# Performance work log

Hardware: AMD Instinct MI355X
Metric: run time of the kernel (lower is better)

The kernel has to match this reference:

```python
import jax, jax.numpy as jnp
import numpy as np

MASK_VALUE = -10000.0


def setup_inputs() -> dict:
    key = jax.random.key(0)
    ks = jax.random.split(key, 6)
    F_, H, L1N, L2N, B = 1024, 2048, 64, 256, 8192

    def w(k, shape, fan_in):
        return jax.random.normal(k, shape, jnp.float32) * (1.0 / np.sqrt(fan_in))

    x = jax.random.normal(ks[0], (B, F_), jnp.float32)
    W1_1 = w(ks[1], (F_, H), F_); b1_1 = jnp.zeros((H,), jnp.float32)
    W1_2 = w(ks[2], (H, L1N), H); b1_2 = jnp.zeros((L1N,), jnp.float32)
    W2_1 = w(ks[3], (F_, H), F_); b2_1 = jnp.zeros((H,), jnp.float32)
    W2_2 = w(ks[4], (2 * H, L2N), 2 * H); b2_2 = jnp.zeros((L2N,), jnp.float32)
    # child_parent[j] = L1 parent of L2 label j (contiguous groups of 4),
    # equivalent to L12_table = [[4i,4i+1,4i+2,4i+3] for i in range(64)]
    child_parent = jnp.arange(L2N, dtype=jnp.int32) // (L2N // L1N)
    return dict(x=x, W1_1=W1_1, b1_1=b1_1, W1_2=W1_2, b1_2=b1_2,
                W2_1=W2_1, b2_1=b2_1, W2_2=W2_2, b2_2=b2_2,
                child_parent=child_parent)


def reference(x, W1_1, b1_1, W1_2, b1_2, W2_1, b2_1, W2_2, b2_2, child_parent):
    h1 = jax.nn.relu(x @ W1_1 + b1_1)          # [B, H]
    h2 = jax.nn.relu(x @ W2_1 + b2_1)          # [B, H]
    cat = jnp.concatenate([h1, h2], axis=1)    # [B, 2H]
    L1 = jax.nn.softmax(jax.nn.relu(h1 @ W1_2 + b1_2), axis=1)   # [B, L1N]
    l2_logits = jax.nn.relu(cat @ W2_2 + b2_2)                   # [B, L2N]
    parent = jnp.argmax(L1, axis=1)                              # [B] int
    # mask[i, j] = 0 if L2 label j is a child of argmax L1 label, else MASK_VALUE
    mask = jnp.where(child_parent[None, :] == parent[:, None], 0.0, MASK_VALUE)
    L2 = jax.nn.softmax(l2_logits + mask, axis=1)
    return (L1, L2)
```

## Files before the change

kernel.cpp:

```cpp
#include <hip/hip_runtime.h>
#include <hip/hip_bf16.h>
#include <stdint.h>
#include <math.h>


typedef _Float16 f16x8 __attribute__((ext_vector_type(8)));
typedef _Float16 f16x4 __attribute__((ext_vector_type(4)));
typedef float    f32x4 __attribute__((ext_vector_type(4)));
typedef unsigned short u16x4 __attribute__((ext_vector_type(4)));

#define MASK_VALUE (-10000.0f)
#define SWZ(r) ((((r) + ((r) >> 2))) & 3)
#define SW4(row, c) ((c) ^ (((row) >> 1) & 3))
#define RSCALE 2048.0f
#define INV_RSCALE (1.0f / 2048.0f)

#define GLOBAL_AS __attribute__((address_space(1)))
#define LDS_AS    __attribute__((address_space(3)))

__device__ __forceinline__ void gload16(const void* g, void* lds) {
    __builtin_amdgcn_global_load_lds((const GLOBAL_AS void*)g, (LDS_AS void*)lds, 16, 0, 0);
}

__device__ __forceinline__ float rd_any(const void* p, size_t i, int flag) {
    return flag ? (float)((const __hip_bfloat16*)p)[i] : ((const float*)p)[i];
}

__device__ __forceinline__ void wg_bar() {
    asm volatile("" ::: "memory");
    __builtin_amdgcn_s_barrier();
    asm volatile("" ::: "memory");
}
#define LGKMN(n) do { asm volatile("s_waitcnt lgkmcnt(" #n ")" ::: "memory"); \
                      __builtin_amdgcn_sched_barrier(0); } while (0)
#define VMW(n)  asm volatile("s_waitcnt vmcnt(" #n ")" ::: "memory")
#define SB0()   __builtin_amdgcn_sched_barrier(0)
#define MFMA16(a,b,c) __builtin_amdgcn_mfma_f32_16x16x32_f16((a),(b),(c),0,0,0)

__global__ void detect_dtype(const unsigned int* __restrict__ x, int* __restrict__ flag) {
    __shared__ int cnt;
    if (threadIdx.x == 0) cnt = 0;
    __syncthreads();
    int local = 0;
#pragma unroll
    for (int i = 0; i < 4; ++i) {
        unsigned int w = x[threadIdx.x * 4 + i];
        unsigned int e = (w >> 7) & 0xFFu;
        if (e >= 96u && e <= 144u) local++;
    }
    atomicAdd(&cnt, local);
    __syncthreads();
    if (threadIdx.x == 0) *flag = (cnt >= 600) ? 1 : 0;
}

__global__ void prep_all(
    const void* __restrict__ x, const void* __restrict__ W1_1,
    const void* __restrict__ W2_1, const void* __restrict__ W2_2,
    const void* __restrict__ W1_2,
    _Float16* __restrict__ xh, _Float16* __restrict__ xl,
    _Float16* __restrict__ whT, _Float16* __restrict__ wlT,
    _Float16* __restrict__ W2Tf, _Float16* __restrict__ W22Tf,
    _Float16* __restrict__ w12h, _Float16* __restrict__ w12l,
    const int* __restrict__ flagp)
{
    __shared__ __align__(16) float tile[64][65];
    int flag = *flagp;
    int bid = blockIdx.x, t = threadIdx.x;
    int tx = t & 63, ty = t >> 6;

    if (bid < 8192) {
        size_t i = ((size_t)bid * 256 + t) * 4;
        float a0, a1, a2, a3;
        if (flag) {
            u16x4 u = *(const u16x4*)((const unsigned short*)x + i);
            a0 = __uint_as_float(((unsigned)u[0]) << 16);
            a1 = __uint_as_float(((unsigned)u[1]) << 16);
            a2 = __uint_as_float(((unsigned)u[2]) << 16);
            a3 = __uint_as_float(((unsigned)u[3]) << 16);
        } else {
            f32x4 f = *(const f32x4*)((const float*)x + i);
            a0 = f[0]; a1 = f[1]; a2 = f[2]; a3 = f[3];
        }
        f16x4 hv, lv;
        _Float16 h0 = (_Float16)a0; hv[0] = h0; lv[0] = (_Float16)((a0 - (float)h0) * RSCALE);
        _Float16 h1 = (_Float16)a1; hv[1] = h1; lv[1] = (_Float16)((a1 - (float)h1) * RSCALE);
        _Float16 h2 = (_Float16)a2; hv[2] = h2; lv[2] = (_Float16)((a2 - (float)h2) * RSCALE);
        _Float16 h3 = (_Float16)a3; hv[3] = h3; lv[3] = (_Float16)((a3 - (float)h3) * RSCALE);
        *(f16x4*)(xh + i) = hv;
        *(f16x4*)(xl + i) = lv;
        return;
    }

    if (bid < 8704) {
        int b = bid - 8192;
        int c0 = (b & 31) * 64, r0 = (b >> 5) * 64;
#pragma unroll
        for (int i = 0; i < 16; ++i) {
            int r = ty + i * 4;
            tile[r][tx] = rd_any(W1_1, (size_t)(r0 + r) * 2048 + c0 + tx, flag);
        }
        __syncthreads();
#pragma unroll
        for (int i = 0; i < 16; ++i) {
            int r = ty + i * 4;
            size_t o = (size_t)(c0 + r) * 1024 + r0 + tx;
            float a = tile[tx][r];
            _Float16 h = (_Float16)a;
            whT[o] = h;
            wlT[o] = (_Float16)((a - (float)h) * RSCALE);
        }
        return;
    }

    if (bid < 9216) {
        int b = bid - 8704;
        int c0 = (b & 31) * 64, r0 = (b >> 5) * 64;
#pragma unroll
        for (int i = 0; i < 16; ++i) {
            int r = ty + i * 4;
            tile[r][tx] = rd_any(W2_1, (size_t)(r0 + r) * 2048 + c0 + tx, flag);
        }
        __syncthreads();
#pragma unroll
        for (int i = 0; i < 16; ++i) {
            int r = ty + i * 4;
            W2Tf[(size_t)(c0 + r) * 1024 + r0 + tx] = (_Float16)tile[tx][r];
        }
        return;
    }

    if (bid < 9472) {
        int b = bid - 9216;
        int c0 = (b & 3) * 64, r0 = (b >> 2) * 64;
#pragma unroll
        for (int i = 0; i < 16; ++i) {
            int r = ty + i * 4;
            tile[r][tx] = rd_any(W2_2, (size_t)(r0 + r) * 256 + c0 + tx, flag);
        }
        __syncthreads();
#pragma unroll
        for (int i = 0; i < 16; ++i) {
            int r = ty + i * 4;
            W22Tf[(size_t)(c0 + r) * 4096 + r0 + tx] = (_Float16)tile[tx][r];
        }
        return;
    }

    {
        int b = bid - 9472;
        int r0 = b * 64;
#pragma unroll
        for (int i = 0; i < 16; ++i) {
            int r = ty + i * 4;
            tile[r][tx] = rd_any(W1_2, (size_t)(r0 + r) * 64 + tx, flag);
        }
        __syncthreads();
#pragma unroll
        for (int i = 0; i < 16; ++i) {
            int r = ty + i * 4;
            size_t o = (size_t)r * 2048 + r0 + tx;
            float a = tile[tx][r];
            _Float16 h = (_Float16)a;
            w12h[o] = h;
            w12l[o] = (_Float16)((a - (float)h) * RSCALE);
        }
    }
}

__global__ __launch_bounds__(512, 2) void h12_gemm8(
    const _Float16* __restrict__ xh, const _Float16* __restrict__ xl,
    const _Float16* __restrict__ whT, const _Float16* __restrict__ wlT,
    const void* __restrict__ b11,
    const _Float16* __restrict__ W2Tf, const void* __restrict__ b21,
    _Float16* __restrict__ h1h, _Float16* __restrict__ h1l,
    _Float16* __restrict__ h2b,
    const int* __restrict__ flagp)
{
    __shared__ __align__(16) char smem[147456];
    int flag = *flagp;
    int t = threadIdx.x, w = t >> 6, lane = t & 63;
    int ml = lane & 15, q = lane >> 4, rq = q * 4;

    int xcd = blockIdx.x & 7, rblk = blockIdx.x >> 3;

    if (rblk < 64) {
        int lb = xcd * 64 + rblk;
        int mt = lb >> 4, nt = lb & 15;
        int i0 = mt * 256, j0 = nt * 128;
        int wr = w & 3, wc = w >> 2;

        f32x4 acc1[4][4], acc2[4][4];
#pragma unroll
        for (int a = 0; a < 4; ++a)
#pragma unroll
            for (int b = 0; b < 4; ++b) {
                acc1[a][b] = (f32x4){0.f, 0.f, 0.f, 0.f};
                acc2[a][b] = (f32x4){0.f, 0.f, 0.f, 0.f};
            }

        f16x8 ah[4], al[4], bh[4], bl[4];

        auto stage = [&](char* bp, int kt, int g) {
            if (g < 4) {
                int ci = ((g & 1) << 9) + t;
                int row = ci >> 2;
                int c = SW4(row, ci & 3);
                const _Float16* src = (g < 2) ? xh : xl;
                gload16(src + (size_t)(i0 + row) * 1024 + kt + c * 8,
                        bp + ((g < 2) ? 0 : 16384) + ci * 16);
            } else {
                int ci = t;
                int row = ci >> 2;
                int c = SW4(row, ci & 3);
                const _Float16* src = (g == 4) ? whT : wlT;
                gload16(src + (size_t)(j0 + row) * 1024 + kt + c * 8,
                        bp + ((g == 4) ? 32768 : 40960) + ci * 16);
            }
        };
        auto rdBA = [&](char* bp) {
#pragma unroll
            for (int ct = 0; ct < 2; ++ct) {
                int row = wc * 64 + ct * 16 + ml;
                int off = row * 64 + (SW4(row, q) << 4);
                bh[ct] = *(const f16x8*)(bp + 32768 + off);
                bl[ct] = *(const f16x8*)(bp + 40960 + off);
            }
        };
        auto rdBB = [&](char* bp) {
#pragma unroll
            for (int ct = 2; ct < 4; ++ct) {
                int row = wc * 64 + ct * 16 + ml;
                int off = row * 64 + (SW4(row, q) << 4);
                bh[ct] = *(const f16x8*)(bp + 32768 + off);
                bl[ct] = *(const f16x8*)(bp + 40960 + off);
            }
        };
        auto rdAlow = [&](char* bp) {
#pragma unroll
            for (int rt = 0; rt < 2; ++rt) {
                int row = wr * 64 + rt * 16 + ml;
                int off = row * 64 + (SW4(row, q) << 4);
                ah[rt] = *(const f16x8*)(bp + off);
                al[rt] = *(const f16x8*)(bp + 16384 + off);
            }
        };
        auto rdAhigh = [&](char* bp) {
#pragma unroll
            for (int rt = 2; rt < 4; ++rt) {
                int row = wr * 64 + rt * 16 + ml;
                int off = row * 64 + (SW4(row, q) << 4);
                ah[rt] = *(const f16x8*)(bp + off);
                al[rt] = *(const f16x8*)(bp + 16384 + off);
            }
        };

#pragma unroll
        for (int g = 0; g < 6; ++g) stage(smem, 0, g);
#pragma unroll
        for (int g = 0; g < 6; ++g) stage(smem + 49152, 32, g);
        VMW(6);
        wg_bar();
        rdBA(smem);   SB0();
        rdAlow(smem); SB0();
        rdBB(smem);   SB0();

        int cur = 0;
        for (int s = 0; s < 32; ++s) {
            char* bpc = smem + cur * 49152;
            char* bpn = smem + ((cur + 1 == 3) ? 0 : cur + 1) * 49152;
            int cur2 = cur + 2; if (cur2 >= 3) cur2 -= 3;
            char* bp2 = smem + cur2 * 49152;
            int kt2 = (s + 2) * 32;
            bool st = (s < 30), rd = (s < 31);

            if (st) {
#pragma unroll
                for (int g = 0; g < 6; ++g) stage(bp2, kt2, g);
            }
            rdAhigh(bpc);
            LGKMN(4);
            __builtin_amdgcn_s_setprio(1);
#pragma unroll
            for (int rt = 0; rt < 2; ++rt)
#pragma unroll
                for (int ct = 0; ct < 4; ++ct) {
                    acc1[rt][ct] = MFMA16(ah[rt], bh[ct], acc1[rt][ct]);
                    acc2[rt][ct] = MFMA16(ah[rt], bl[ct], acc2[rt][ct]);
                    acc2[rt][ct] = MFMA16(al[rt], bh[ct], acc2[rt][ct]);
                }
            __builtin_amdgcn_s_setprio(0);
            LGKMN(0);
            __builtin_amdgcn_s_setprio(1);
#pragma unroll
            for (int rt = 2; rt < 4; ++rt)
#pragma unroll
                for (int ct = 0; ct < 2; ++ct) {
                    acc1[rt][ct] = MFMA16(ah[rt], bh[ct], acc1[rt][ct]);
                    acc2[rt][ct] = MFMA16(ah[rt], bl[ct], acc2[rt][ct]);
                    acc2[rt][ct] = MFMA16(al[rt], bh[ct], acc2[rt][ct]);
                }
            __builtin_amdgcn_s_setprio(0);
            if (st) { VMW(6); } else { VMW(0); }
            wg_bar();
            if (rd) { rdBA(bpn); rdAlow(bpn); }
            SB0();
            __builtin_amdgcn_s_setprio(1);
#pragma unroll
            for (int rt = 2; rt < 4; ++rt)
#pragma unroll
                for (int ct = 2; ct < 4; ++ct) {
                    acc1[rt][ct] = MFMA16(ah[rt], bh[ct], acc1[rt][ct]);
                    acc2[rt][ct] = MFMA16(ah[rt], bl[ct], acc2[rt][ct]);
                    acc2[rt][ct] = MFMA16(al[rt], bh[ct], acc2[rt][ct]);
                }
            __builtin_amdgcn_s_setprio(0);
            if (rd) rdBB(bpn);
            SB0();
            cur = cur + 1; if (cur == 3) cur = 0;
        }

#pragma unroll
        for (int ct = 0; ct < 4; ++ct) {
            float bv = rd_any(b11, j0 + wc * 64 + ct * 16 + ml, flag);
#pragma unroll
            for (int rt = 0; rt < 4; ++rt)
#pragma unroll
                for (int rr = 0; rr < 4; ++rr) {
                    float v = acc1[rt][ct][rr] + acc2[rt][ct][rr] * INV_RSCALE + bv;
                    acc1[rt][ct][rr] = v > 0.f ? v : 0.f;
                }
        }
        _Float16* C = (_Float16*)smem;
#pragma unroll
        for (int p = 0; p < 2; ++p) {
            __syncthreads();
#pragma unroll
            for (int rt = 0; rt < 4; ++rt)
#pragma unroll
                for (int ct = 0; ct < 4; ++ct)
#pragma unroll
                    for (int rr = 0; rr < 4; ++rr) {
                        float v = acc1[rt][ct][rr];
                        _Float16 h = (_Float16)v;
                        _Float16 outv = (p == 0) ? h
                                      : (_Float16)((v - (float)h) * RSCALE);
                        int rl = wr * 64 + rt * 16 + rq + rr;
                        int cl = wc * 64 + ct * 16 + ml;
                        C[rl * 136 + cl] = outv;
                    }
            __syncthreads();
            _Float16* dst = (p == 0) ? h1h : h1l;
#pragma unroll
            for (int i = 0; i < 8; ++i) {
                int c = i * 512 + t;
                int row = c >> 4, c8 = (c & 15) * 8;
                *(f16x8*)(dst + (size_t)(i0 + row) * 2048 + j0 + c8) =
                    *(const f16x8*)(C + row * 136 + c8);
            }
        }
    } else {
        int lb = xcd * 32 + (rblk - 64);
        int mt = lb >> 3, nt = lb & 7;
        int i0 = mt * 256, j0 = nt * 256;
        int wr = w & 1, wc = w >> 1;

        f32x4 acc[8][4];
#pragma unroll
        for (int a = 0; a < 8; ++a)
#pragma unroll
            for (int b = 0; b < 4; ++b) acc[a][b] = (f32x4){0.f, 0.f, 0.f, 0.f};

        f16x8 af0[4], af4[4], bfa[4], bfb[4];

        auto stage = [&](char* bp, int kt, int g) {
            int ci = ((g & 1) << 9) + t;
            int row = ci >> 2;
            int c = SW4(row, ci & 3);
            if (g < 2)
                gload16(xh + (size_t)(i0 + row) * 1024 + kt + c * 8,
                        bp + ci * 16);
            else
                gload16(W2Tf + (size_t)(j0 + row) * 1024 + kt + c * 8,
                        bp + 16384 + ci * 16);
        };
        auto rdBF = [&](char* bp, f16x8* dst) {
#pragma unroll
            for (int ct = 0; ct < 4; ++ct) {
                int row = wc * 64 + ct * 16 + ml;
                int off = row * 64 + (SW4(row, q) << 4);
                dst[ct] = *(const f16x8*)(bp + 16384 + off);
            }
        };
        auto rdA0 = [&](char* bp) {
#pragma unroll
            for (int rt = 0; rt < 4; ++rt) {
                int row = wr * 128 + rt * 16 + ml;
                int off = row * 64 + (SW4(row, q) << 4);
                af0[rt] = *(const f16x8*)(bp + off);
            }
        };
        auto rdA4 = [&](char* bp) {
#pragma unroll
            for (int rt = 0; rt < 4; ++rt) {
                int row = wr * 128 + (rt + 4) * 16 + ml;
                int off = row * 64 + (SW4(row, q) << 4);
                af4[rt] = *(const f16x8*)(bp + off);
            }
        };

#pragma unroll
        for (int g = 0; g < 4; ++g) stage(smem, 0, g);
#pragma unroll
        for (int g = 0; g < 4; ++g) stage(smem + 32768, 32, g);
        VMW(4);
        wg_bar();
        rdBF(smem, bfa); SB0();
        rdA0(smem);      SB0();
        rdA4(smem);      SB0();

        int cur = 0;
        auto body = [&](int s, f16x8* BFC, f16x8* BFN) {
            char* bpn = smem + ((cur + 1) & 3) * 32768;
            char* bp2 = smem + ((cur + 2) & 3) * 32768;
            int kt2 = (s + 2) * 32;
            bool st = (s < 30), rd = (s < 31);

            if (st) {
#pragma unroll
                for (int g = 0; g < 4; ++g) stage(bp2, kt2, g);
            }
            LGKMN(4);
            __builtin_amdgcn_s_setprio(1);
#pragma unroll
            for (int rt = 0; rt < 4; ++rt)
#pragma unroll
                for (int ct = 0; ct < 4; ++ct)
                    acc[rt][ct] = MFMA16(af0[rt], BFC[ct], acc[rt][ct]);
            __builtin_amdgcn_s_setprio(0);
            LGKMN(0);
            if (st) { VMW(4); } else { VMW(0); }
            wg_bar();
            if (rd) { rdBF(bpn, BFN); rdA0(bpn); }
            SB0();
            __builtin_amdgcn_s_setprio(1);
#pragma unroll
            for (int rt = 0; rt < 4; ++rt)
#pragma unroll
                for (int ct = 0; ct < 4; ++ct)
                    acc[rt + 4][ct] = MFMA16(af4[rt], BFC[ct], acc[rt + 4][ct]);
            __builtin_amdgcn_s_setprio(0);
            if (rd) rdA4(bpn);
            cur = (cur + 1) & 3;
        };

        for (int k = 0; k < 16; ++k) {
            body(2 * k,     bfa, bfb);
            body(2 * k + 1, bfb, bfa);
        }

        _Float16* C = (_Float16*)smem;
        __syncthreads();
#pragma unroll
        for (int ct = 0; ct < 4; ++ct) {
            float bv = rd_any(b21, j0 + wc * 64 + ct * 16 + ml, flag);
#pragma unroll
            for (int rt = 0; rt < 8; ++rt)
#pragma unroll
                for (int rr = 0; rr < 4; ++rr) {
                    float v = acc[rt][ct][rr] + bv;
                    v = v > 0.f ? v : 0.f;
                    int rl = wr * 128 + rt * 16 + rq + rr;
                    int cl = wc * 64 + ct * 16 + ml;
                    C[rl * 264 + cl] = (_Float16)v;
                }
        }
        __syncthreads();
#pragma unroll
        for (int i = 0; i < 16; ++i) {
            int c = i * 512 + t;
            int row = c >> 5, c8 = (c & 31) * 8;
            *(f16x8*)(h2b + (size_t)(i0 + row) * 2048 + j0 + c8) =
                *(const f16x8*)(C + row * 264 + c8);
        }
    }
}

__global__ __launch_bounds__(256, 2) void head_fused(
    const _Float16* __restrict__ h1h, const _Float16* __restrict__ h1l,
    const _Float16* __restrict__ h2b, const _Float16* __restrict__ W22T,
    float* __restrict__ partials,
    const _Float16* __restrict__ w12h, const _Float16* __restrict__ w12l,
    const void* __restrict__ b12, float* __restrict__ L1out,
    int* __restrict__ parent, const int* __restrict__ flagp)
{
    constexpr int BK = 32;
    __shared__ __align__(16) char smem[16384];
    int flag = *flagp;
    int t = threadIdx.x, w = t >> 6, lane = t & 63;
    int ml = lane & 15, q = lane >> 4;

    if (blockIdx.x < 512) {
        _Float16* As = (_Float16*)smem;
        _Float16* Bs = (_Float16*)(smem + 8192);
        int bid = blockIdx.x;
        int g = bid & 7, s = bid >> 3;
        int mt = g * 8 + (s & 7);
        int rest = s >> 3;
        int nt = rest & 1, kc = rest >> 1;
        int i0 = mt * 128, j0 = nt * 128;
        const _Float16* Abase = (kc < 2) ? h1h : h2b;
        int kof = (kc & 1) * 1024;
        int wr = w & 1, wcb = w >> 1;

        f32x4 acc[4][4];
#pragma unroll
        for (int a = 0; a < 4; ++a)
#pragma unroll
            for (int b = 0; b < 4; ++b) acc[a][b] = (f32x4){0.f, 0.f, 0.f, 0.f};

        for (int kt = 0; kt < 1024; kt += BK) {
            __syncthreads();
#pragma unroll
            for (int qq = 0; qq < 2; ++qq) {
                int c = qq * 256 + t;
                int row = c >> 2;
                int gc = (c & 3) ^ SWZ(row);
                gload16(Abase + (size_t)(i0 + row) * 2048 + kof + kt + gc * 8, (char*)As + c * 16);
                gload16(W22T + (size_t)(j0 + row) * 4096 + kc * 1024 + kt + gc * 8, (char*)Bs + c * 16);
            }
            __syncthreads();
            f16x8 af[4], bf[4];
#pragma unroll
            for (int rt = 0; rt < 4; ++rt) {
                int row = wr * 64 + rt * 16 + ml;
                af[rt] = *(const f16x8*)(As + row * 32 + ((q ^ SWZ(row)) << 3));
            }
#pragma unroll
            for (int ct = 0; ct < 4; ++ct) {
                int row = wcb * 64 + ct * 16 + ml;
                bf[ct] = *(const f16x8*)(Bs + row * 32 + ((q ^ SWZ(row)) << 3));
            }
#pragma unroll
            for (int rt = 0; rt < 4; ++rt)
#pragma unroll
                for (int ct = 0; ct < 4; ++ct)
                    acc[rt][ct] = __builtin_amdgcn_mfma_f32_16x16x32_f16(
                        af[rt], bf[ct], acc[rt][ct], 0, 0, 0);
        }

        float* out = partials + (size_t)kc * 8192 * 256;
        int rq = (lane >> 4) * 4;
#pragma unroll
        for (int ct = 0; ct < 4; ++ct) {
            int nl = j0 + wcb * 64 + ct * 16 + ml;
#pragma unroll
            for (int rt = 0; rt < 4; ++rt) {
                int mbase = i0 + wr * 64 + rt * 16 + rq;
#pragma unroll
                for (int r = 0; r < 4; ++r)
                    out[(size_t)(mbase + r) * 256 + nl] = acc[rt][ct][r];
            }
        }
    } else {
        float* red = (float*)smem;
        int r0 = (blockIdx.x - 512) * 16;
        int kq = (lane >> 4) * 8;

        f32x4 acch[4], accx[4];
#pragma unroll
        for (int ct = 0; ct < 4; ++ct) {
            acch[ct] = (f32x4){0.f, 0.f, 0.f, 0.f};
            accx[ct] = (f32x4){0.f, 0.f, 0.f, 0.f};
        }

        size_t aoff = (size_t)(r0 + ml) * 2048 + w * 512 + kq;
        const _Float16* Ah = h1h + aoff;
        const _Float16* Al = h1l + aoff;
        size_t boff[4];
#pragma unroll
        for (int ct = 0; ct < 4; ++ct)
            boff[ct] = (size_t)(ct * 16 + ml) * 2048 + w * 512 + kq;

        f16x8 ah = *(const f16x8*)(Ah), al = *(const f16x8*)(Al);
        f16x8 bh[4], bl[4];
#pragma unroll
        for (int ct = 0; ct < 4; ++ct) {
            bh[ct] = *(const f16x8*)(w12h + boff[ct]);
            bl[ct] = *(const f16x8*)(w12l + boff[ct]);
        }

        for (int kt = 0; kt < 512; kt += 32) {
            int nk = (kt + 32) & 511;
            f16x8 nah = *(const f16x8*)(Ah + nk);
            f16x8 nal = *(const f16x8*)(Al + nk);
            f16x8 nbh[4], nbl[4];
#pragma unroll
            for (int ct = 0; ct < 4; ++ct) {
                nbh[ct] = *(const f16x8*)(w12h + boff[ct] + nk);
                nbl[ct] = *(const f16x8*)(w12l + boff[ct] + nk);
            }
#pragma unroll
            for (int ct = 0; ct < 4; ++ct) {
                acch[ct] = __builtin_amdgcn_mfma_f32_16x16x32_f16(ah, bh[ct], acch[ct], 0, 0, 0);
                accx[ct] = __builtin_amdgcn_mfma_f32_16x16x32_f16(ah, bl[ct], accx[ct], 0, 0, 0);
                accx[ct] = __builtin_amdgcn_mfma_f32_16x16x32_f16(al, bh[ct], accx[ct], 0, 0, 0);
            }
            ah = nah; al = nal;
#pragma unroll
            for (int ct = 0; ct < 4; ++ct) { bh[ct] = nbh[ct]; bl[ct] = nbl[ct]; }
        }

        f32x4 acc[4];
#pragma unroll
        for (int ct = 0; ct < 4; ++ct)
#pragma unroll
            for (int i = 0; i < 4; ++i)
                acc[ct][i] = acch[ct][i] + accx[ct][i] * INV_RSCALE;

        if (w > 0) {
#pragma unroll
            for (int ct = 0; ct < 4; ++ct)
#pragma unroll
                for (int i = 0; i < 4; ++i)
                    red[((w - 1) * 4 + ct) * 256 + lane * 4 + i] = acc[ct][i];
        }
        __syncthreads();
        if (w != 0) return;

#pragma unroll
        for (int wv = 0; wv < 3; ++wv)
#pragma unroll
            for (int ct = 0; ct < 4; ++ct)
#pragma unroll
                for (int i = 0; i < 4; ++i)
                    acc[ct][i] += red[(wv * 4 + ct) * 256 + lane * 4 + i];

        int rq = (lane >> 4) * 4;
        float vals[4][4];
        float vmax[4] = {-1e30f, -1e30f, -1e30f, -1e30f};
        int vidx[4] = {1 << 30, 1 << 30, 1 << 30, 1 << 30};
#pragma unroll
        for (int ct = 0; ct < 4; ++ct) {
            int col = ct * 16 + ml;
            float bv = rd_any(b12, col, flag);
#pragma unroll
            for (int r = 0; r < 4; ++r) {
                float v = acc[ct][r] + bv;
                v = v > 0.f ? v : 0.f;
                vals[ct][r] = v;
                if (v > vmax[r] || (v == vmax[r] && col < vidx[r])) { vmax[r] = v; vidx[r] = col; }
            }
        }
#pragma unroll
        for (int d = 1; d < 16; d <<= 1) {
#pragma unroll
            for (int r = 0; r < 4; ++r) {
                float om = __shfl_xor(vmax[r], d);
                int oi = __shfl_xor(vidx[r], d);
                if (om > vmax[r] || (om == vmax[r] && oi < vidx[r])) { vmax[r] = om; vidx[r] = oi; }
            }
        }
        float vsum[4] = {0.f, 0.f, 0.f, 0.f};
#pragma unroll
        for (int ct = 0; ct < 4; ++ct)
#pragma unroll
            for (int r = 0; r < 4; ++r) {
                float e = __expf(vals[ct][r] - vmax[r]);
                vals[ct][r] = e;
                vsum[r] += e;
            }
#pragma unroll
        for (int d = 1; d < 16; d <<= 1)
#pragma unroll
            for (int r = 0; r < 4; ++r) vsum[r] += __shfl_xor(vsum[r], d);

#pragma unroll
        for (int r = 0; r < 4; ++r) {
            float inv = 1.0f / vsum[r];
            int grow = r0 + rq + r;
#pragma unroll
            for (int ct = 0; ct < 4; ++ct)
                L1out[(size_t)grow * 64 + ct * 16 + ml] = vals[ct][r] * inv;
            if (ml == 0) parent[grow] = vidx[r];
        }
    }
}

__global__ __launch_bounds__(256, 2) void l2_softmax(
    const float* __restrict__ partials, const void* __restrict__ b22,
    const int* __restrict__ child_parent, const int* __restrict__ parent,
    float* __restrict__ L2out, const int* __restrict__ flagp)
{
    int flag = *flagp;
    int t = threadIdx.x, w = t >> 6, lane = t & 63;
    int row = blockIdx.x * 4 + w;
    int c4 = lane * 4;

    float v[4] = {0.f, 0.f, 0.f, 0.f};
#pragma unroll
    for (int kc = 0; kc < 4; ++kc) {
        float4 pv = *(const float4*)(partials + ((size_t)kc * 8192 + row) * 256 + c4);
        v[0] += pv.x; v[1] += pv.y; v[2] += pv.z; v[3] += pv.w;
    }
    int par = parent[row];
#pragma unroll
    for (int j = 0; j < 4; ++j) {
        float x = v[j] + rd_any(b22, c4 + j, flag);
        x = x > 0.f ? x : 0.f;
        if (child_parent[c4 + j] != par) x += MASK_VALUE;
        v[j] = x;
    }
    float m = fmaxf(fmaxf(v[0], v[1]), fmaxf(v[2], v[3]));
#pragma unroll
    for (int d = 1; d < 64; d <<= 1) m = fmaxf(m, __shfl_xor(m, d));
    float sum = 0.f;
#pragma unroll
    for (int j = 0; j < 4; ++j) { v[j] = __expf(v[j] - m); sum += v[j]; }
#pragma unroll
    for (int d = 1; d < 64; d <<= 1) sum += __shfl_xor(sum, d);
    float inv = 1.0f / sum;
    float4 o = {v[0] * inv, v[1] * inv, v[2] * inv, v[3] * inv};
    *(float4*)(L2out + (size_t)row * 256 + c4) = o;
}

extern "C" void kernel_launch(void* const* d_in, const int* in_sizes, int n_in,
                              void* d_out, int out_size, void* d_ws, size_t ws_size,
                              hipStream_t stream) {
    (void)in_sizes; (void)n_in; (void)out_size; (void)ws_size;

    const void* x    = d_in[0];
    const void* W1_1 = d_in[1];
    const void* b1_1 = d_in[2];
    const void* W1_2 = d_in[3];
    const void* b1_2 = d_in[4];
    const void* W2_1 = d_in[5];
    const void* b2_1 = d_in[6];
    const void* W2_2 = d_in[7];
    const void* b2_2 = d_in[8];
    const int* child_parent = (const int*)d_in[9];

    char* p = (char*)d_ws;
    _Float16* xh    = (_Float16*)(p);
    _Float16* xl    = (_Float16*)(p + 16777216);
    _Float16* whT   = (_Float16*)(p + 33554432);
    _Float16* wlT   = (_Float16*)(p + 37748736);
    _Float16* h1h   = (_Float16*)(p + 41943040);
    _Float16* h1l   = (_Float16*)(p + 75497472);
    _Float16* h2b   = (_Float16*)(p + 109051904);
    _Float16* W2Tf  = (_Float16*)(p + 142606336);
    _Float16* W22Tf = (_Float16*)(p + 146800640);
    _Float16* w12h  = (_Float16*)(p + 148897792);
    _Float16* w12l  = (_Float16*)(p + 149159936);
    float* partials = (float*)(p + 149422080);
    int* parent     = (int*)(p + 182976512);
    int* flag       = (int*)(p + 183009280);

    float* L1out = (float*)d_out;
    float* L2out = L1out + (size_t)8192 * 64;

    hipLaunchKernelGGL(detect_dtype, dim3(1), dim3(256), 0, stream,
                       (const unsigned int*)x, flag);
    hipLaunchKernelGGL(prep_all, dim3(9504), dim3(256), 0, stream,
                       x, W1_1, W2_1, W2_2, W1_2,
                       xh, xl, whT, wlT, W2Tf, W22Tf, w12h, w12l, flag);
    hipLaunchKernelGGL(h12_gemm8, dim3(768), dim3(512), 0, stream,
                       xh, xl, whT, wlT, b1_1, W2Tf, b2_1,
                       h1h, h1l, h2b, flag);
    hipLaunchKernelGGL(head_fused, dim3(1024), dim3(256), 0, stream,
                       h1h, h1l, h2b, W22Tf, partials,
                       w12h, w12l, b1_2, L1out, parent, flag);
    hipLaunchKernelGGL(l2_softmax, dim3(2048), dim3(256), 0, stream,
                       partials, b2_2, child_parent, parent, L2out, flag);
}
```

Baseline: 319.1 us.

## Split head kernel into pipelined L2 GEMM and separate L1 head kernel

Replaces the combined head kernel with two launches. The L2 GEMM now uses 512-thread blocks, each covering a 128x256 output tile, with a triple-buffered LDS pipeline (global_load_lds prefetch two stages ahead), XCD-aware block mapping and an interleaved MFMA/LDS-read schedule using s_setprio. The L1 head becomes its own kernel. This aims to hide global load latency and raise MFMA utilisation, at the cost of an extra kernel launch and the loss of overlap between the L1 and L2 heads.

```diff
diff --git a/kernel.cpp b/kernel.cpp
--- a/kernel.cpp
+++ b/kernel.cpp
@@ -485,204 +485,262 @@
     }
 }
 
-__global__ __launch_bounds__(256, 2) void head_fused(
+__global__ __launch_bounds__(512, 2) void l2_gemm(
+    const _Float16* __restrict__ h1h, const _Float16* __restrict__ h2b,
+    const _Float16* __restrict__ W22T, float* __restrict__ partials)
+{
+    __shared__ __align__(16) char smem[73728];
+    int t = threadIdx.x, w = t >> 6, lane = t & 63;
+    int ml = lane & 15, q = lane >> 4, rq = q * 4;
+    int wr = w & 1, wc = w >> 1;
+
+    int xcd = blockIdx.x & 7, r = blockIdx.x >> 3;
+    int lb = xcd * 32 + r;
+    int kc = lb >> 6, mt = lb & 63;
+    int i0 = mt * 128;
+    const _Float16* Abase = (kc < 2) ? h1h : h2b;
+    int kof = (kc & 1) * 1024;
+
+    f32x4 acc[4][4];
+#pragma unroll
+    for (int a = 0; a < 4; ++a)
+#pragma unroll
+        for (int b = 0; b < 4; ++b) acc[a][b] = (f32x4){0.f, 0.f, 0.f, 0.f};
+
+    f16x8 af0[2], af4[2], bfa[4], bfb[4];
+
+    auto stage = [&](char* bp, int kt) {
+        {
+            int ci = t;
+            int row = ci >> 2;
+            int c = SW4(row, ci & 3);
+            gload16(Abase + (size_t)(i0 + row) * 2048 + kof + kt + c * 8,
+                    bp + ci * 16);
+        }
+#pragma unroll
+        for (int g = 0; g < 2; ++g) {
+            int ci = (g << 9) + t;
+            int row = ci >> 2;
+            int c = SW4(row, ci & 3);
+            gload16(W22T + (size_t)row * 4096 + kc * 1024 + kt + c * 8,
+                    bp + 8192 + ci * 16);
+        }
+    };
+    auto rdBF = [&](char* bp, f16x8* dst) {
+#pragma unroll
+        for (int ct = 0; ct < 4; ++ct) {
+            int row = wc * 64 + ct * 16 + ml;
+            int off = row * 64 + (SW4(row, q) << 4);
+            dst[ct] = *(const f16x8*)(bp + 8192 + off);
+        }
+    };
+    auto rdA0 = [&](char* bp) {
+#pragma unroll
+        for (int rt = 0; rt < 2; ++rt) {
+            int row = wr * 64 + rt * 16 + ml;
+            int off = row * 64 + (SW4(row, q) << 4);
+            af0[rt] = *(const f16x8*)(bp + off);
+        }
+    };
+    auto rdA4 = [&](char* bp) {
+#pragma unroll
+        for (int rt = 0; rt < 2; ++rt) {
+            int row = wr * 64 + (rt + 2) * 16 + ml;
+            int off = row * 64 + (SW4(row, q) << 4);
+            af4[rt] = *(const f16x8*)(bp + off);
+        }
+    };
+
+    stage(smem, 0);
+    stage(smem + 24576, 32);
+    VMW(3);
+    wg_bar();
+    rdBF(smem, bfa); SB0();
+    rdA0(smem);      SB0();
+    rdA4(smem);      SB0();
+
+    int cur = 0;
+    auto body = [&](int s, f16x8* BFC, f16x8* BFN) {
+        char* bpn = smem + ((cur + 1 == 3) ? 0 : cur + 1) * 24576;
+        int cur2 = cur + 2; if (cur2 >= 3) cur2 -= 3;
+        char* bp2 = smem + cur2 * 24576;
+        int kt2 = (s + 2) * 32;
+        bool st = (s < 30), rd = (s < 31);
+
+        if (st) stage(bp2, kt2);
+        LGKMN(2);
+        __builtin_amdgcn_s_setprio(1);
+#pragma unroll
+        for (int rt = 0; rt < 2; ++rt)
+#pragma unroll
+            for (int ct = 0; ct < 4; ++ct)
+                acc[rt][ct] = MFMA16(af0[rt], BFC[ct], acc[rt][ct]);
+        __builtin_amdgcn_s_setprio(0);
+        LGKMN(0);
+        if (st) { VMW(3); } else { VMW(0); }
+        wg_bar();
+        if (rd) { rdBF(bpn, BFN); rdA0(bpn); }
+        SB0();
+        __builtin_amdgcn_s_setprio(1);
+#pragma unroll
+        for (int rt = 0; rt < 2; ++rt)
+#pragma unroll
+            for (int ct = 0; ct < 4; ++ct)
+                acc[rt + 2][ct] = MFMA16(af4[rt], BFC[ct], acc[rt + 2][ct]);
+        __builtin_amdgcn_s_setprio(0);
+        if (rd) rdA4(bpn);
+        SB0();
+        cur = cur + 1; if (cur == 3) cur = 0;
+    };
+
+    for (int k = 0; k < 16; ++k) {
+        body(2 * k,     bfa, bfb);
+        body(2 * k + 1, bfb, bfa);
+    }
+
+    float* out = partials + (size_t)kc * 8192 * 256;
+#pragma unroll
+    for (int ct = 0; ct < 4; ++ct) {
+        int nl = wc * 64 + ct * 16 + ml;
+#pragma unroll
+        for (int rt = 0; rt < 4; ++rt) {
+            int mbase = i0 + wr * 64 + rt * 16 + rq;
+#pragma unroll
+            for (int rr = 0; rr < 4; ++rr)
+                out[(size_t)(mbase + rr) * 256 + nl] = acc[rt][ct][rr];
+        }
+    }
+}
+
+__global__ __launch_bounds__(256, 2) void l1_head(
     const _Float16* __restrict__ h1h, const _Float16* __restrict__ h1l,
-    const _Float16* __restrict__ h2b, const _Float16* __restrict__ W22T,
-    float* __restrict__ partials,
     const _Float16* __restrict__ w12h, const _Float16* __restrict__ w12l,
     const void* __restrict__ b12, float* __restrict__ L1out,
     int* __restrict__ parent, const int* __restrict__ flagp)
 {
-    constexpr int BK = 32;
-    __shared__ __align__(16) char smem[16384];
+    __shared__ __align__(16) float red[3072];
     int flag = *flagp;
     int t = threadIdx.x, w = t >> 6, lane = t & 63;
-    int ml = lane & 15, q = lane >> 4;
-
-    if (blockIdx.x < 512) {
-        _Float16* As = (_Float16*)smem;
-        _Float16* Bs = (_Float16*)(smem + 8192);
-        int bid = blockIdx.x;
-        int g = bid & 7, s = bid >> 3;
-        int mt = g * 8 + (s & 7);
-        int rest = s >> 3;
-        int nt = rest & 1, kc = rest >> 1;
-        int i0 = mt * 128, j0 = nt * 128;
-        const _Float16* Abase = (kc < 2) ? h1h : h2b;
-        int kof = (kc & 1) * 1024;
-        int wr = w & 1, wcb = w >> 1;
-
-        f32x4 acc[4][4];
-#pragma unroll
-        for (int a = 0; a < 4; ++a)
-#pragma unroll
-            for (int b = 0; b < 4; ++b) acc[a][b] = (f32x4){0.f, 0.f, 0.f, 0.f};
-
-        for (int kt = 0; kt < 1024; kt += BK) {
-            __syncthreads();
-#pragma unroll
-            for (int qq = 0; qq < 2; ++qq) {
-                int c = qq * 256 + t;
-                int row = c >> 2;
-                int gc = (c & 3) ^ SWZ(row);
-                gload16(Abase + (size_t)(i0 + row) * 2048 + kof + kt + gc * 8, (char*)As + c * 16);
-                gload16(W22T + (size_t)(j0 + row) * 4096 + kc * 1024 + kt + gc * 8, (char*)Bs + c * 16);
-            }
-            __syncthreads();
-            f16x8 af[4], bf[4];
-#pragma unroll
-            for (int rt = 0; rt < 4; ++rt) {
-                int row = wr * 64 + rt * 16 + ml;
-                af[rt] = *(const f16x8*)(As + row * 32 + ((q ^ SWZ(row)) << 3));
-            }
-#pragma unroll
-            for (int ct = 0; ct < 4; ++ct) {
-                int row = wcb * 64 + ct * 16 + ml;
-                bf[ct] = *(const f16x8*)(Bs + row * 32 + ((q ^ SWZ(row)) << 3));
-            }
-#pragma unroll
-            for (int rt = 0; rt < 4; ++rt)
-#pragma unroll
-                for (int ct = 0; ct < 4; ++ct)
-                    acc[rt][ct] = __builtin_amdgcn_mfma_f32_16x16x32_f16(
-                        af[rt], bf[ct], acc[rt][ct], 0, 0, 0);
-        }
-
-        float* out = partials + (size_t)kc * 8192 * 256;
-        int rq = (lane >> 4) * 4;
+    int ml = lane & 15;
+    int r0 = blockIdx.x * 16;
+    int kq = (lane >> 4) * 8;
+
+    f32x4 acch[4], accx[4];
+#pragma unroll
+    for (int ct = 0; ct < 4; ++ct) {
+        acch[ct] = (f32x4){0.f, 0.f, 0.f, 0.f};
+        accx[ct] = (f32x4){0.f, 0.f, 0.f, 0.f};
+    }
+
+    size_t aoff = (size_t)(r0 + ml) * 2048 + w * 512 + kq;
+    const _Float16* Ah = h1h + aoff;
+    const _Float16* Al = h1l + aoff;
+    size_t boff[4];
+#pragma unroll
+    for (int ct = 0; ct < 4; ++ct)
+        boff[ct] = (size_t)(ct * 16 + ml) * 2048 + w * 512 + kq;
+
+    f16x8 ah = *(const f16x8*)(Ah), al = *(const f16x8*)(Al);
+    f16x8 bh[4], bl[4];
+#pragma unroll
+    for (int ct = 0; ct < 4; ++ct) {
+        bh[ct] = *(const f16x8*)(w12h + boff[ct]);
+        bl[ct] = *(const f16x8*)(w12l + boff[ct]);
+    }
+
+    for (int kt = 0; kt < 512; kt += 32) {
+        int nk = (kt + 32) & 511;
+        f16x8 nah = *(const f16x8*)(Ah + nk);
+        f16x8 nal = *(const f16x8*)(Al + nk);
+        f16x8 nbh[4], nbl[4];
 #pragma unroll
         for (int ct = 0; ct < 4; ++ct) {
-            int nl = j0 + wcb * 64 + ct * 16 + ml;
-#pragma unroll
-            for (int rt = 0; rt < 4; ++rt) {
-                int mbase = i0 + wr * 64 + rt * 16 + rq;
-#pragma unroll
-                for (int r = 0; r < 4; ++r)
-                    out[(size_t)(mbase + r) * 256 + nl] = acc[rt][ct][r];
-            }
-        }
-    } else {
-        float* red = (float*)smem;
-        int r0 = (blockIdx.x - 512) * 16;
-        int kq = (lane >> 4) * 8;
-
-        f32x4 acch[4], accx[4];
+            nbh[ct] = *(const f16x8*)(w12h + boff[ct] + nk);
+            nbl[ct] = *(const f16x8*)(w12l + boff[ct] + nk);
+        }
 #pragma unroll
         for (int ct = 0; ct < 4; ++ct) {
-            acch[ct] = (f32x4){0.f, 0.f, 0.f, 0.f};
-            accx[ct] = (f32x4){0.f, 0.f, 0.f, 0.f};
-        }
-
-        size_t aoff = (size_t)(r0 + ml) * 2048 + w * 512 + kq;
-        const _Float16* Ah = h1h + aoff;
-        const _Float16* Al = h1l + aoff;
-        size_t boff[4];
+            acch[ct] = __builtin_amdgcn_mfma_f32_16x16x32_f16(ah, bh[ct], acch[ct], 0, 0, 0);
+            accx[ct] = __builtin_amdgcn_mfma_f32_16x16x32_f16(ah, bl[ct], accx[ct], 0, 0, 0);
+            accx[ct] = __builtin_amdgcn_mfma_f32_16x16x32_f16(al, bh[ct], accx[ct], 0, 0, 0);
+        }
+        ah = nah; al = nal;
+#pragma unroll
+        for (int ct = 0; ct < 4; ++ct) { bh[ct] = nbh[ct]; bl[ct] = nbl[ct]; }
+    }
+
+    f32x4 acc[4];
+#pragma unroll
+    for (int ct = 0; ct < 4; ++ct)
+#pragma unroll
+        for (int i = 0; i < 4; ++i)
+            acc[ct][i] = acch[ct][i] + accx[ct][i] * INV_RSCALE;
+
+    if (w > 0) {
 #pragma unroll
         for (int ct = 0; ct < 4; ++ct)
-            boff[ct] = (size_t)(ct * 16 + ml) * 2048 + w * 512 + kq;
-
-        f16x8 ah = *(const f16x8*)(Ah), al = *(const f16x8*)(Al);
-        f16x8 bh[4], bl[4];
-#pragma unroll
-        for (int ct = 0; ct < 4; ++ct) {
-            bh[ct] = *(const f16x8*)(w12h + boff[ct]);
-            bl[ct] = *(const f16x8*)(w12l + boff[ct]);
-        }
-
-        for (int kt = 0; kt < 512; kt += 32) {
-            int nk = (kt + 32) & 511;
-            f16x8 nah = *(const f16x8*)(Ah + nk);
-            f16x8 nal = *(const f16x8*)(Al + nk);
-            f16x8 nbh[4], nbl[4];
-#pragma unroll
-            for (int ct = 0; ct < 4; ++ct) {
-                nbh[ct] = *(const f16x8*)(w12h + boff[ct] + nk);
-                nbl[ct] = *(const f16x8*)(w12l + boff[ct] + nk);
-            }
-#pragma unroll
-            for (int ct = 0; ct < 4; ++ct) {
-                acch[ct] = __builtin_amdgcn_mfma_f32_16x16x32_f16(ah, bh[ct], acch[ct], 0, 0, 0);
-                accx[ct] = __builtin_amdgcn_mfma_f32_16x16x32_f16(ah, bl[ct], accx[ct], 0, 0, 0);
-                accx[ct] = __builtin_amdgcn_mfma_f32_16x16x32_f16(al, bh[ct], accx[ct], 0, 0, 0);
-            }
-            ah = nah; al = nal;
-#pragma unroll
-            for (int ct = 0; ct < 4; ++ct) { bh[ct] = nbh[ct]; bl[ct] = nbl[ct]; }
-        }
-
-        f32x4 acc[4];
+#pragma unroll
+            for (int i = 0; i < 4; ++i)
+                red[((w - 1) * 4 + ct) * 256 + lane * 4 + i] = acc[ct][i];
+    }
+    __syncthreads();
+    if (w != 0) return;
+
+#pragma unroll
+    for (int wv = 0; wv < 3; ++wv)
 #pragma unroll
         for (int ct = 0; ct < 4; ++ct)
 #pragma unroll
             for (int i = 0; i < 4; ++i)
-                acc[ct][i] = acch[ct][i] + accx[ct][i] * INV_RSCALE;
-
-        if (w > 0) {
-#pragma unroll
-            for (int ct = 0; ct < 4; ++ct)
-#pragma unroll
-                for (int i = 0; i < 4; ++i)
-                    red[((w - 1) * 4 + ct) * 256 + lane * 4 + i] = acc[ct][i];
-        }
-        __syncthreads();
-        if (w != 0) return;
-
-#pragma unroll
-        for (int wv = 0; wv < 3; ++wv)
-#pragma unroll
-            for (int ct = 0; ct < 4; ++ct)
-#pragma unroll
-                for (int i = 0; i < 4; ++i)
-                    acc[ct][i] += red[(wv * 4 + ct) * 256 + lane * 4 + i];
-
-        int rq = (lane >> 4) * 4;
-        float vals[4][4];
-        float vmax[4] = {-1e30f, -1e30f, -1e30f, -1e30f};
-        int vidx[4] = {1 << 30, 1 << 30, 1 << 30, 1 << 30};
-#pragma unroll
-        for (int ct = 0; ct < 4; ++ct) {
-            int col = ct * 16 + ml;
-            float bv = rd_any(b12, col, flag);
-#pragma unroll
-            for (int r = 0; r < 4; ++r) {
-                float v = acc[ct][r] + bv;
-                v = v > 0.f ? v : 0.f;
-                vals[ct][r] = v;
-                if (v > vmax[r] || (v == vmax[r] && col < vidx[r])) { vmax[r] = v; vidx[r] = col; }
-            }
-        }
-#pragma unroll
-        for (int d = 1; d < 16; d <<= 1) {
-#pragma unroll
-            for (int r = 0; r < 4; ++r) {
-                float om = __shfl_xor(vmax[r], d);
-                int oi = __shfl_xor(vidx[r], d);
-                if (om > vmax[r] || (om == vmax[r] && oi < vidx[r])) { vmax[r] = om; vidx[r] = oi; }
-            }
-        }
-        float vsum[4] = {0.f, 0.f, 0.f, 0.f};
+                acc[ct][i] += red[(wv * 4 + ct) * 256 + lane * 4 + i];
+
+    int rq = (lane >> 4) * 4;
+    float vals[4][4];
+    float vmax[4] = {-1e30f, -1e30f, -1e30f, -1e30f};
+    int vidx[4] = {1 << 30, 1 << 30, 1 << 30, 1 << 30};
+#pragma unroll
+    for (int ct = 0; ct < 4; ++ct) {
+        int col = ct * 16 + ml;
+        float bv = rd_any(b12, col, flag);
+#pragma unroll
+        for (int rr = 0; rr < 4; ++rr) {
+            float v = acc[ct][rr] + bv;
+            v = v > 0.f ? v : 0.f;
+            vals[ct][rr] = v;
+            if (v > vmax[rr] || (v == vmax[rr] && col < vidx[rr])) { vmax[rr] = v; vidx[rr] = col; }
+        }
+    }
+#pragma unroll
+    for (int d = 1; d < 16; d <<= 1) {
+#pragma unroll
+        for (int rr = 0; rr < 4; ++rr) {
+            float om = __shfl_xor(vmax[rr], d);
+            int oi = __shfl_xor(vidx[rr], d);
+            if (om > vmax[rr] || (om == vmax[rr] && oi < vidx[rr])) { vmax[rr] = om; vidx[rr] = oi; }
+        }
+    }
+    float vsum[4] = {0.f, 0.f, 0.f, 0.f};
+#pragma unroll
+    for (int ct = 0; ct < 4; ++ct)
+#pragma unroll
+        for (int rr = 0; rr < 4; ++rr) {
+            float e = __expf(vals[ct][rr] - vmax[rr]);
+            vals[ct][rr] = e;
+            vsum[rr] += e;
+        }
+#pragma unroll
+    for (int d = 1; d < 16; d <<= 1)
+#pragma unroll
+        for (int rr = 0; rr < 4; ++rr) vsum[rr] += __shfl_xor(vsum[rr], d);
+
+#pragma unroll
+    for (int rr = 0; rr < 4; ++rr) {
+        float inv = 1.0f / vsum[rr];
+        int grow = r0 + rq + rr;
 #pragma unroll
         for (int ct = 0; ct < 4; ++ct)
-#pragma unroll
-            for (int r = 0; r < 4; ++r) {
-                float e = __expf(vals[ct][r] - vmax[r]);
-                vals[ct][r] = e;
-                vsum[r] += e;
-            }
-#pragma unroll
-        for (int d = 1; d < 16; d <<= 1)
-#pragma unroll
-            for (int r = 0; r < 4; ++r) vsum[r] += __shfl_xor(vsum[r], d);
-
-#pragma unroll
-        for (int r = 0; r < 4; ++r) {
-            float inv = 1.0f / vsum[r];
-            int grow = r0 + rq + r;
-#pragma unroll
-            for (int ct = 0; ct < 4; ++ct)
-                L1out[(size_t)grow * 64 + ct * 16 + ml] = vals[ct][r] * inv;
-            if (ml == 0) parent[grow] = vidx[r];
-        }
+            L1out[(size_t)grow * 64 + ct * 16 + ml] = vals[ct][rr] * inv;
+        if (ml == 0) parent[grow] = vidx[rr];
     }
 }
 
@@ -766,9 +824,10 @@
     hipLaunchKernelGGL(h12_gemm8, dim3(768), dim3(512), 0, stream,
                        xh, xl, whT, wlT, b1_1, W2Tf, b2_1,
                        h1h, h1l, h2b, flag);
-    hipLaunchKernelGGL(head_fused, dim3(1024), dim3(256), 0, stream,
-                       h1h, h1l, h2b, W22Tf, partials,
-                       w12h, w12l, b1_2, L1out, parent, flag);
+    hipLaunchKernelGGL(l2_gemm, dim3(256), dim3(512), 0, stream,
+                       h1h, h2b, W22Tf, partials);
+    hipLaunchKernelGGL(l1_head, dim3(512), dim3(256), 0, stream,
+                       h1h, h1l, w12h, w12l, b1_2, L1out, parent, flag);
     hipLaunchKernelGGL(l2_softmax, dim3(2048), dim3(256), 0, stream,
                        partials, b2_2, child_parent, parent, L2out, flag);
 }
```

Measured after the change: 327.3 us. 1.03x slower.
